# Performance work log

Measured on AMD Instinct MI355X. Metric: run time of the kernel, lower is better.

The kernel has to match this reference:

```python
import jax, jax.numpy as jnp
import numpy as np

S, N, D, F, E = 2048, 8, 1024, 4096, 8
STD = 0.02


def setup_inputs() -> dict:
    key = jax.random.key(0)
    ks = jax.random.split(key, 5)
    x = jax.random.normal(ks[0], (S, N, D), dtype=jnp.float32)
    Wg = jax.random.normal(ks[1], (E, D), dtype=jnp.float32) * STD
    W1 = jax.random.normal(ks[2], (E, F, D), dtype=jnp.float32) * STD
    b1 = jnp.zeros((E, F), dtype=jnp.float32)
    W2 = jax.random.normal(ks[3], (E, D, F), dtype=jnp.float32) * STD
    b2 = jnp.zeros((E, D), dtype=jnp.float32)
    return {"x": x, "Wg": Wg, "W1": W1, "b1": b1, "W2": W2, "b2": b2}


def reference(x, Wg, W1, b1, W2, b2):
    # Gate (eval mode: no gating noise). scores: [S, N, E]
    scores = jnp.einsum('snd,ed->sne', x, Wg)
    prob = jax.nn.softmax(scores, axis=-1)
    top1_idx = jnp.argmax(prob, axis=-1)                                   # [S, N] int
    top1_prob = jnp.take_along_axis(prob, top1_idx[..., None], axis=-1)[..., 0]  # [S, N]

    y = jnp.zeros_like(x)
    n_experts = Wg.shape[0]
    for e in range(n_experts):  # small fixed loop over experts
        h = jax.nn.gelu(jnp.einsum('snd,fd->snf', x, W1[e]) + b1[e], approximate=False)
        ye = jnp.einsum('snf,df->snd', h, W2[e]) + b2[e]
        mask = (top1_idx == e)[..., None]                                  # [S, N, 1]
        y = y + jnp.where(mask, ye * top1_prob[..., None], 0.0)
    return y
```

## Files before the change

kernel.cpp:

```cpp
#include <hip/hip_runtime.h>

#define S_TOK 16384
#define D_DIM 1024
#define F_DIM 4096
#define E_NUM 8

#define BM 128
#define BN 128
#define BK 32

typedef short bf16x8 __attribute__((ext_vector_type(8)));
typedef float f32x4 __attribute__((ext_vector_type(4)));
typedef unsigned short ushort_t;

static __device__ __forceinline__ unsigned short f32_bf16(float f) {
  unsigned u = __float_as_uint(f);
  return (unsigned short)((u + 0x7FFFu + ((u >> 16) & 1u)) >> 16);
}

static __device__ __forceinline__ unsigned int pack_bf16x2(float a, float b) {
  unsigned ua = __float_as_uint(a);
  unsigned ub = __float_as_uint(b);
  unsigned lo = (ua + 0x7FFFu + ((ua >> 16) & 1u)) >> 16;
  unsigned hi = (ub + 0x7FFFu + ((ub >> 16) & 1u)) & 0xFFFF0000u;
  return lo | hi;
}

static __device__ __forceinline__ uint2 cvt_f4_bf4(const float4 v) {
  uint2 r;
  r.x = pack_bf16x2(v.x, v.y);
  r.y = pack_bf16x2(v.z, v.w);
  return r;
}

static __device__ __forceinline__ void load_lds16(const void* g, void* l) {
  __builtin_amdgcn_global_load_lds(g, l, 16, 0, 0);
}

__global__ void zero_counts_kernel(int* counts) {
  if (threadIdx.x < E_NUM) counts[threadIdx.x] = 0;
}

__global__ void cast_kernel(const float* __restrict__ in, ushort_t* __restrict__ out) {
  const size_t base = ((size_t)blockIdx.x * blockDim.x + threadIdx.x) * 8;
  const float4 v0 = *(const float4*)(in + base);
  const float4 v1 = *(const float4*)(in + base + 4);
  const uint2 a = cvt_f4_bf4(v0), b = cvt_f4_bf4(v1);
  uint4 w; w.x = a.x; w.y = a.y; w.z = b.x; w.w = b.y;
  *(uint4*)(out + base) = w;
}

__global__ void gate_kernel(const float* __restrict__ x,
                            const float* __restrict__ Wg,
                            ushort_t* __restrict__ xbf,
                            float* __restrict__ prob,
                            int* __restrict__ counts,
                            int* __restrict__ tok_list) {
  const int wv = threadIdx.x >> 6;
  const int lane = threadIdx.x & 63;
  const int t = blockIdx.x * 4 + wv;
  const float* xr = x + (size_t)t * D_DIM;
  ushort_t* xb = xbf + (size_t)t * D_DIM;

  float acc[E_NUM];
#pragma unroll
  for (int e = 0; e < E_NUM; ++e) acc[e] = 0.0f;

#pragma unroll
  for (int i = 0; i < 4; ++i) {
    const int k = i * 256 + lane * 4;
    const float4 v = *(const float4*)(xr + k);
    *(uint2*)(xb + k) = cvt_f4_bf4(v);
#pragma unroll
    for (int e = 0; e < E_NUM; ++e) {
      const float4 w = *(const float4*)(Wg + e * D_DIM + k);
      acc[e] += v.x * w.x + v.y * w.y + v.z * w.z + v.w * w.w;
    }
  }
#pragma unroll
  for (int e = 0; e < E_NUM; ++e) {
#pragma unroll
    for (int off = 32; off > 0; off >>= 1)
      acc[e] += __shfl_xor(acc[e], off, 64);
  }
  if (lane == 0) {
    float m = acc[0]; int bi = 0;
#pragma unroll
    for (int e = 1; e < E_NUM; ++e) {
      if (acc[e] > m) { m = acc[e]; bi = e; }
    }
    float s = 0.0f;
#pragma unroll
    for (int e = 0; e < E_NUM; ++e) s += expf(acc[e] - m);
    prob[t] = 1.0f / s;
    int p = atomicAdd(&counts[bi], 1);
    tok_list[bi * S_TOK + p] = t;
  }
}

template <int KDIM, int NDIM, int EPI>
__global__ void ffn_kernel(const ushort_t* __restrict__ A,
                           const ushort_t* __restrict__ B,
                           const float* __restrict__ bias,
                           const float* __restrict__ prob,
                           const int* __restrict__ counts,
                           const int* __restrict__ tok_list,
                           ushort_t* __restrict__ Hout,
                           float* __restrict__ out) {
  const int e = blockIdx.z;
  const int cnt = counts[e];
  const int m0 = blockIdx.y * BM;
  if (m0 >= cnt) return;
  const int n0 = blockIdx.x * BN;

  __shared__ ushort_t As[BM * BK];
  __shared__ ushort_t Bs[BN * BK];

  const int tid = threadIdx.x;
  const int lane = tid & 63;
  const int w = tid >> 6;
  const int wr = (w >> 1) * 64;
  const int wc = (w & 1) * 64;

  const int r0 = tid >> 2;
  const int r1 = 64 + r0;
  const int cb = (tid & 3) * 8;

  const size_t ebase = (size_t)e * S_TOK;
  const int tokA0 = (m0 + r0 < cnt) ? tok_list[ebase + m0 + r0] : 0;
  const int tokA1 = (m0 + r1 < cnt) ? tok_list[ebase + m0 + r1] : 0;
  const ushort_t* pA0 = A + (size_t)tokA0 * KDIM + cb;
  const ushort_t* pA1 = A + (size_t)tokA1 * KDIM + cb;
  const ushort_t* Be = B + (size_t)e * NDIM * KDIM;
  const ushort_t* pB0 = Be + (size_t)(n0 + r0) * KDIM + cb;
  const ushort_t* pB1 = Be + (size_t)(n0 + r1) * KDIM + cb;

  ushort_t* lA0 = &As[w * 512];
  ushort_t* lA1 = &As[2048 + w * 512];
  ushort_t* lB0 = &Bs[w * 512];
  ushort_t* lB1 = &Bs[2048 + w * 512];

  f32x4 acc[4][4];
#pragma unroll
  for (int i = 0; i < 4; ++i)
#pragma unroll
    for (int j = 0; j < 4; ++j)
      acc[i][j] = (f32x4){0.f, 0.f, 0.f, 0.f};

  for (int k0 = 0; k0 < KDIM; k0 += BK) {
    load_lds16(pA0 + k0, lA0);
    load_lds16(pA1 + k0, lA1);
    load_lds16(pB0 + k0, lB0);
    load_lds16(pB1 + k0, lB1);
    __syncthreads();

    const ushort_t* Ab = &As[(wr + (lane & 15)) * BK + (lane >> 4) * 8];
    const ushort_t* Bb = &Bs[(wc + (lane & 15)) * BK + (lane >> 4) * 8];
    bf16x8 a[4], b[4];
#pragma unroll
    for (int i = 0; i < 4; ++i) {
      a[i] = *(const bf16x8*)(Ab + i * 16 * BK);
      b[i] = *(const bf16x8*)(Bb + i * 16 * BK);
    }
#pragma unroll
    for (int mi = 0; mi < 4; ++mi)
#pragma unroll
      for (int ni = 0; ni < 4; ++ni)
        acc[mi][ni] = __builtin_amdgcn_mfma_f32_16x16x32_bf16(a[mi], b[ni], acc[mi][ni], 0, 0, 0);
    __syncthreads();
  }

  const float* be = bias + (size_t)e * NDIM;
#pragma unroll
  for (int mi = 0; mi < 4; ++mi) {
#pragma unroll
    for (int r = 0; r < 4; ++r) {
      const int slot = m0 + wr + mi * 16 + ((lane >> 4) * 4) + r;
      if (slot >= cnt) continue;
      const int tok = tok_list[ebase + slot];
      if (EPI == 0) {
        ushort_t* hrow = Hout + (size_t)tok * NDIM;
#pragma unroll
        for (int ni = 0; ni < 4; ++ni) {
          const int col = n0 + wc + ni * 16 + (lane & 15);
          float v = acc[mi][ni][r] + be[col];
          v = 0.5f * v * (1.0f + erff(v * 0.70710678118654752f));
          hrow[col] = f32_bf16(v);
        }
      } else {
        const float p = prob[tok];
        float* orow = out + (size_t)tok * NDIM;
#pragma unroll
        for (int ni = 0; ni < 4; ++ni) {
          const int col = n0 + wc + ni * 16 + (lane & 15);
          orow[col] = (acc[mi][ni][r] + be[col]) * p;
        }
      }
    }
  }
}

extern "C" void kernel_launch(void* const* d_in, const int* in_sizes, int n_in,
                              void* d_out, int out_size, void* d_ws, size_t ws_size,
                              hipStream_t stream) {
  const float* x  = (const float*)d_in[0];
  const float* Wg = (const float*)d_in[1];
  const float* W1 = (const float*)d_in[2];
  const float* b1 = (const float*)d_in[3];
  const float* W2 = (const float*)d_in[4];
  const float* b2 = (const float*)d_in[5];
  float* out = (float*)d_out;

  const size_t MB = 1ull << 20;
  char* ws = (char*)d_ws;
  int* counts      = (int*)(ws);
  float* prob      = (float*)(ws + 64 * 1024);
  int* tok_list    = (int*)(ws + 128 * 1024);
  ushort_t* xbf    = (ushort_t*)(ws + 1 * MB);
  ushort_t* W1bf   = (ushort_t*)(ws + 33 * MB);
  ushort_t* W2bf   = (ushort_t*)(ws + 97 * MB);
  ushort_t* H      = (ushort_t*)(ws + 161 * MB);

  zero_counts_kernel<<<1, 64, 0, stream>>>(counts);
  gate_kernel<<<S_TOK / 4, 256, 0, stream>>>(x, Wg, xbf, prob, counts, tok_list);

  cast_kernel<<<16384, 256, 0, stream>>>(W1, W1bf);
  cast_kernel<<<16384, 256, 0, stream>>>(W2, W2bf);

  dim3 g1(F_DIM / BN, S_TOK / BM, E_NUM);
  ffn_kernel<D_DIM, F_DIM, 0><<<g1, 256, 0, stream>>>(xbf, W1bf, b1, nullptr, counts, tok_list, H, nullptr);

  dim3 g2(D_DIM / BN, S_TOK / BM, E_NUM);
  ffn_kernel<F_DIM, D_DIM, 1><<<g2, 256, 0, stream>>>(H, W2bf, b2, prob, counts, tok_list, nullptr, out);
}
```

Before: 791.9 us.

## Compact expert tile schedule, double-buffer LDS, and add launch bounds

Measured after the change: 780.5 us. Within noise of the previous version (-1.4%).

```diff
diff --git a/kernel.cpp b/kernel.cpp
--- a/kernel.cpp
+++ b/kernel.cpp
@@ -8,6 +8,7 @@
 #define BM 128
 #define BN 128
 #define BK 32
+#define NTILES_MAX 136
 
 typedef short bf16x8 __attribute__((ext_vector_type(8)));
 typedef float f32x4 __attribute__((ext_vector_type(4)));
@@ -98,23 +99,45 @@
   }
 }
 
+__global__ void plan_kernel(const int* __restrict__ counts, int* __restrict__ plan) {
+  if (threadIdx.x == 0) {
+    int t = 0;
+    for (int e = 0; e < E_NUM; ++e) {
+      const int nt = (counts[e] + BM - 1) / BM;
+      for (int i = 0; i < nt; ++i) {
+        plan[1 + t] = e;
+        plan[1 + NTILES_MAX + t] = i * BM;
+        ++t;
+      }
+    }
+    plan[0] = t;
+  }
+}
+
 template <int KDIM, int NDIM, int EPI>
+__launch_bounds__(256, 4)
 __global__ void ffn_kernel(const ushort_t* __restrict__ A,
                            const ushort_t* __restrict__ B,
                            const float* __restrict__ bias,
                            const float* __restrict__ prob,
                            const int* __restrict__ counts,
                            const int* __restrict__ tok_list,
+                           const int* __restrict__ plan,
                            ushort_t* __restrict__ Hout,
                            float* __restrict__ out) {
-  const int e = blockIdx.z;
+  constexpr int NT = NDIM / BN;
+  constexpr int NWG = NT * NTILES_MAX;
+  const int ntiles = plan[0];
+  const int wg = (blockIdx.x & 7) * (NWG >> 3) + (blockIdx.x >> 3);
+  const int tile = wg / NT;
+  if (tile >= ntiles) return;
+  const int n0 = (wg % NT) * BN;
+  const int e = plan[1 + tile];
+  const int m0 = plan[1 + NTILES_MAX + tile];
   const int cnt = counts[e];
-  const int m0 = blockIdx.y * BM;
-  if (m0 >= cnt) return;
-  const int n0 = blockIdx.x * BN;
-
-  __shared__ ushort_t As[BM * BK];
-  __shared__ ushort_t Bs[BN * BK];
+
+  __shared__ ushort_t As[2][BM * BK];
+  __shared__ ushort_t Bs[2][BM * BK];
 
   const int tid = threadIdx.x;
   const int lane = tid & 63;
@@ -135,11 +158,6 @@
   const ushort_t* pB0 = Be + (size_t)(n0 + r0) * KDIM + cb;
   const ushort_t* pB1 = Be + (size_t)(n0 + r1) * KDIM + cb;
 
-  ushort_t* lA0 = &As[w * 512];
-  ushort_t* lA1 = &As[2048 + w * 512];
-  ushort_t* lB0 = &Bs[w * 512];
-  ushort_t* lB1 = &Bs[2048 + w * 512];
-
   f32x4 acc[4][4];
 #pragma unroll
   for (int i = 0; i < 4; ++i)
@@ -147,15 +165,27 @@
     for (int j = 0; j < 4; ++j)
       acc[i][j] = (f32x4){0.f, 0.f, 0.f, 0.f};
 
-  for (int k0 = 0; k0 < KDIM; k0 += BK) {
-    load_lds16(pA0 + k0, lA0);
-    load_lds16(pA1 + k0, lA1);
-    load_lds16(pB0 + k0, lB0);
-    load_lds16(pB1 + k0, lB1);
-    __syncthreads();
-
-    const ushort_t* Ab = &As[(wr + (lane & 15)) * BK + (lane >> 4) * 8];
-    const ushort_t* Bb = &Bs[(wc + (lane & 15)) * BK + (lane >> 4) * 8];
+  constexpr int NK = KDIM / BK;
+
+  load_lds16(pA0, &As[0][w * 512]);
+  load_lds16(pA1, &As[0][2048 + w * 512]);
+  load_lds16(pB0, &Bs[0][w * 512]);
+  load_lds16(pB1, &Bs[0][2048 + w * 512]);
+  __syncthreads();
+
+  int cur = 0;
+  for (int t = 0; t < NK; ++t) {
+    if (t + 1 < NK) {
+      const int k0 = (t + 1) * BK;
+      const int nb = cur ^ 1;
+      load_lds16(pA0 + k0, &As[nb][w * 512]);
+      load_lds16(pA1 + k0, &As[nb][2048 + w * 512]);
+      load_lds16(pB0 + k0, &Bs[nb][w * 512]);
+      load_lds16(pB1 + k0, &Bs[nb][2048 + w * 512]);
+    }
+
+    const ushort_t* Ab = &As[cur][(wr + (lane & 15)) * BK + (lane >> 4) * 8];
+    const ushort_t* Bb = &Bs[cur][(wc + (lane & 15)) * BK + (lane >> 4) * 8];
     bf16x8 a[4], b[4];
 #pragma unroll
     for (int i = 0; i < 4; ++i) {
@@ -167,7 +197,9 @@
 #pragma unroll
       for (int ni = 0; ni < 4; ++ni)
         acc[mi][ni] = __builtin_amdgcn_mfma_f32_16x16x32_bf16(a[mi], b[ni], acc[mi][ni], 0, 0, 0);
+
     __syncthreads();
+    cur ^= 1;
   }
 
   const float* be = bias + (size_t)e * NDIM;
@@ -214,6 +246,7 @@
   const size_t MB = 1ull << 20;
   char* ws = (char*)d_ws;
   int* counts      = (int*)(ws);
+  int* plan        = (int*)(ws + 4096);
   float* prob      = (float*)(ws + 64 * 1024);
   int* tok_list    = (int*)(ws + 128 * 1024);
   ushort_t* xbf    = (ushort_t*)(ws + 1 * MB);
@@ -223,13 +256,14 @@
 
   zero_counts_kernel<<<1, 64, 0, stream>>>(counts);
   gate_kernel<<<S_TOK / 4, 256, 0, stream>>>(x, Wg, xbf, prob, counts, tok_list);
+  plan_kernel<<<1, 64, 0, stream>>>(counts, plan);
 
   cast_kernel<<<16384, 256, 0, stream>>>(W1, W1bf);
   cast_kernel<<<16384, 256, 0, stream>>>(W2, W2bf);
 
-  dim3 g1(F_DIM / BN, S_TOK / BM, E_NUM);
-  ffn_kernel<D_DIM, F_DIM, 0><<<g1, 256, 0, stream>>>(xbf, W1bf, b1, nullptr, counts, tok_list, H, nullptr);
-
-  dim3 g2(D_DIM / BN, S_TOK / BM, E_NUM);
-  ffn_kernel<F_DIM, D_DIM, 1><<<g2, 256, 0, stream>>>(H, W2bf, b2, prob, counts, tok_list, nullptr, out);
-}
+  ffn_kernel<D_DIM, F_DIM, 0><<<(F_DIM / BN) * NTILES_MAX, 256, 0, stream>>>(
+      xbf, W1bf, b1, nullptr, counts, tok_list, plan, H, nullptr);
+
+  ffn_kernel<F_DIM, D_DIM, 1><<<(D_DIM / BN) * NTILES_MAX, 256, 0, stream>>>(
+      H, W2bf, b2, prob, counts, tok_list, plan, nullptr, out);
+}
```
